# Optimization experiments

Hardware: AMD Instinct MI355X
Metric: run time of the kernel (lower is better)

The kernel has to match this reference:

```python
import jax, jax.numpy as jnp
import numpy as np

MARGIN = 0.5  # init kwarg margin=0.5 (float -> fix_margin branch)

N, D, NUM_CLASSES = 8192, 128, 512


def setup_inputs() -> dict:
    key = jax.random.key(0)
    k1, k2 = jax.random.split(key)
    embeds = jax.random.normal(k1, (N, D), dtype=jnp.float32)
    labels = jax.random.randint(k2, (N,), 0, NUM_CLASSES)
    return {"embeds": embeds, "labels": labels}


def reference(embeds, labels):
    n = embeds.shape[0]
    # --- batch-hard mining (detached in original: .detach().cpu().numpy()) ---
    # Euclidean pairwise distances via Gram trick (avoids [N,N,D] intermediate).
    sq = jnp.sum(embeds * embeds, axis=1)  # [N]
    d2 = sq[:, None] + sq[None, :] - 2.0 * (embeds @ embeds.T)  # [N,N]
    dist = jnp.sqrt(jnp.maximum(d2, 0.0))
    dist = jax.lax.stop_gradient(dist)

    same = labels[:, None] == labels[None, :]  # [N,N]
    eye = jnp.eye(n, dtype=bool)
    pos_mask = same & ~eye          # same label, not self
    neg_mask = ~same                # different label (diag excluded since same there)

    pos_idx = jnp.argmax(jnp.where(pos_mask, dist, -jnp.inf), axis=1)  # hardest positive
    neg_idx = jnp.argmin(jnp.where(neg_mask, dist, jnp.inf), axis=1)   # hardest negative

    # --- margin loss with metric='sqeuclidean' (gradients flow through gathers) ---
    dp = embeds - embeds[pos_idx]
    dn = embeds - embeds[neg_idx]
    ap = jnp.sum(dp * dp, axis=1)
    an = jnp.sum(dn * dn, axis=1)
    return jnp.mean(jax.nn.relu(ap - an + MARGIN))
```

## Files before the change

### kernel.cpp

```cpp
#include <hip/hip_runtime.h>
#include <stdint.h>

#define NROWS 8192
#define DIM 128
#define MARGIN 0.5f

typedef short short8 __attribute__((ext_vector_type(8)));
typedef float f32x4 __attribute__((ext_vector_type(4)));
typedef int   int4v __attribute__((ext_vector_type(4)));

static __device__ __forceinline__ unsigned short f2bf(float f) {
    union { float f; unsigned u; } x; x.f = f;
    unsigned u = x.u;
    return (unsigned short)((u + 0x7FFFu + ((u >> 16) & 1u)) >> 16);
}

__global__ __launch_bounds__(256) void prep(const float* __restrict__ emb,
                                            char* __restrict__ efrag,
                                            float* __restrict__ cbuf,
                                            unsigned* __restrict__ pos,
                                            unsigned* __restrict__ neg,
                                            float* __restrict__ out) {
    const int d = threadIdx.x & 63;
    const int row = blockIdx.x * 4 + (threadIdx.x >> 6);
    const float2 v = reinterpret_cast<const float2*>(emb + row * DIM)[d];
    float sq = v.x * v.x + v.y * v.y;
#pragma unroll
    for (int m = 1; m < 64; m <<= 1) sq += __shfl_xor(sq, m, 64);
    const unsigned pack = ((unsigned)f2bf(v.y) << 16) | (unsigned)f2bf(v.x);
    char* dst = efrag + (size_t)(row >> 4) * 4096 + (d >> 4) * 1024
              + ((((d >> 2) & 3) * 16 + (row & 15)) * 16) + (d & 3) * 4;
    *reinterpret_cast<unsigned*>(dst) = pack;
    if (d == 0) cbuf[row] = sq + 512.0f;
    if (d == 1) pos[row] = 0u;
    if (d == 2) neg[row] = 0xFFFFFFFFu;
    if (blockIdx.x == 0 && threadIdx.x == 0) out[0] = 0.0f;
}

__global__ __launch_bounds__(256, 4) void mine(const char* __restrict__ efrag,
                                               const float* __restrict__ cbuf,
                                               const int* __restrict__ labels,
                                               unsigned* __restrict__ pos,
                                               unsigned* __restrict__ neg) {
    const int tid  = threadIdx.x;
    const int wave = tid >> 6;
    const int lane = tid & 63;
    const int l15  = lane & 15;
    const int lhi  = lane >> 4;
    const int iblk = blockIdx.x & 31;
    const int cblk = blockIdx.x >> 5;
    const int ibase = iblk * 256 + wave * 64;

    short8 bfrag[4][4];
    int labi[4];
#pragma unroll
    for (int it = 0; it < 4; ++it) {
        const char* bt = efrag + (size_t)((ibase >> 4) + it) * 4096 + lane * 16;
#pragma unroll
        for (int ks = 0; ks < 4; ++ks)
            bfrag[it][ks] = *reinterpret_cast<const short8*>(bt + ks * 1024);
        labi[it] = labels[ibase + it * 16 + l15];
    }

    unsigned bp[4] = {0u, 0u, 0u, 0u};
    unsigned bn[4] = {0xFFFFFFFFu, 0xFFFFFFFFu, 0xFFFFFFFFu, 0xFFFFFFFFu};

    const int jc = cblk * 256;
    const char* aj = efrag + (size_t)(cblk * 16) * 4096 + lane * 16;

#pragma unroll 2
    for (int jt = 0; jt < 16; ++jt) {
        const int jb = jc + jt * 16;
        const int4v labj = *reinterpret_cast<const int4v*>(labels + jb + lhi * 4);
        const f32x4 cinit = *reinterpret_cast<const f32x4*>(cbuf + jb + lhi * 4) * -0.5f;
        const char* at = aj + (size_t)jt * 4096;

        const short8 af0 = *reinterpret_cast<const short8*>(at);
        const short8 af1 = *reinterpret_cast<const short8*>(at + 1024);
        f32x4 acc[4];
#pragma unroll
        for (int it = 0; it < 4; ++it)
            acc[it] = __builtin_amdgcn_mfma_f32_16x16x32_bf16(af0, bfrag[it][0], cinit, 0, 0, 0);
#pragma unroll
        for (int it = 0; it < 4; ++it)
            acc[it] = __builtin_amdgcn_mfma_f32_16x16x32_bf16(af1, bfrag[it][1], acc[it], 0, 0, 0);
        const short8 af2 = *reinterpret_cast<const short8*>(at + 2048);
        const short8 af3 = *reinterpret_cast<const short8*>(at + 3072);
#pragma unroll
        for (int it = 0; it < 4; ++it)
            acc[it] = __builtin_amdgcn_mfma_f32_16x16x32_bf16(af2, bfrag[it][2], acc[it], 0, 0, 0);
#pragma unroll
        for (int it = 0; it < 4; ++it)
            acc[it] = __builtin_amdgcn_mfma_f32_16x16x32_bf16(af3, bfrag[it][3], acc[it], 0, 0, 0);

        const int jv = jb + lhi * 4;
#pragma unroll
        for (int it = 0; it < 4; ++it) {
#pragma unroll
            for (int r = 0; r < 4; ++r) {
                union { float f; unsigned u; } cv; cv.f = acc[it][r];
                const unsigned cand = (cv.u & 0xFFFFE000u) | (unsigned)(jv + r);
                const bool eq = (labj[r] == labi[it]);
                const unsigned psel = eq ? cand : 0u;
                const unsigned nsel = eq ? 0xFFFFFFFFu : cand;
                bp[it] = bp[it] > psel ? bp[it] : psel;
                bn[it] = bn[it] < nsel ? bn[it] : nsel;
            }
        }
    }

#pragma unroll
    for (int it = 0; it < 4; ++it) {
        unsigned o;
        o = (unsigned)__shfl_xor((int)bp[it], 16, 64); bp[it] = bp[it] > o ? bp[it] : o;
        o = (unsigned)__shfl_xor((int)bp[it], 32, 64); bp[it] = bp[it] > o ? bp[it] : o;
        o = (unsigned)__shfl_xor((int)bn[it], 16, 64); bn[it] = bn[it] < o ? bn[it] : o;
        o = (unsigned)__shfl_xor((int)bn[it], 32, 64); bn[it] = bn[it] < o ? bn[it] : o;
        if (lane < 16) {
            const int i = ibase + it * 16 + lane;
            atomicMax(&pos[i], bp[it]);
            atomicMin(&neg[i], bn[it]);
        }
    }
}

__global__ __launch_bounds__(256) void lossk(const float* __restrict__ emb,
                                             const unsigned* __restrict__ pos,
                                             const unsigned* __restrict__ neg,
                                             float* __restrict__ bsum) {
    __shared__ float wsum[4];
    const int tid = threadIdx.x, lane = tid & 63, wave = tid >> 6;
    const int i = blockIdx.x * 4 + wave;
    const int jp = (int)(pos[i] & 8191u);
    const int jn = (int)(neg[i] & 8191u);
    const float2 a = reinterpret_cast<const float2*>(emb + (size_t)i  * DIM)[lane];
    const float2 b = reinterpret_cast<const float2*>(emb + (size_t)jp * DIM)[lane];
    const float2 c = reinterpret_cast<const float2*>(emb + (size_t)jn * DIM)[lane];
    float dx = a.x - b.x, dy = a.y - b.y;
    const float ap = dx * dx + dy * dy;
    dx = a.x - c.x; dy = a.y - c.y;
    const float an = dx * dx + dy * dy;
    float s = ap - an;
#pragma unroll
    for (int m = 1; m < 64; m <<= 1) s += __shfl_xor(s, m, 64);
    if (lane == 0) wsum[wave] = fmaxf(s + MARGIN, 0.f);
    __syncthreads();
    if (tid == 0) bsum[blockIdx.x] = wsum[0] + wsum[1] + wsum[2] + wsum[3];
}

__global__ __launch_bounds__(256) void fin(const float* __restrict__ bsum,
                                           float* __restrict__ out) {
    __shared__ float wsum[4];
    const int tid = threadIdx.x, lane = tid & 63, wave = tid >> 6;
    float s = 0.f;
#pragma unroll
    for (int k = 0; k < 8; ++k) s += bsum[tid + k * 256];
#pragma unroll
    for (int m = 1; m < 64; m <<= 1) s += __shfl_xor(s, m, 64);
    if (lane == 0) wsum[wave] = s;
    __syncthreads();
    if (tid == 0) out[0] = (wsum[0] + wsum[1] + wsum[2] + wsum[3]) * (1.0f / (float)NROWS);
}

extern "C" void kernel_launch(void* const* d_in, const int* in_sizes, int n_in,
                              void* d_out, int out_size, void* d_ws, size_t ws_size,
                              hipStream_t stream) {
    const float* emb   = (const float*)d_in[0];
    const int* labels  = (const int*)d_in[1];
    float* out = (float*)d_out;
    char* ws = (char*)d_ws;

    char* efrag    = ws;
    float* cbuf    = (float*)(ws + (size_t)2097152);
    unsigned* pos  = (unsigned*)(ws + (size_t)2097152 + 32768);
    unsigned* neg  = pos + NROWS;
    float* bsum    = (float*)(neg + NROWS);

    prep<<<2048, 256, 0, stream>>>(emb, efrag, cbuf, pos, neg, out);
    mine<<<1024, 256, 0, stream>>>(efrag, cbuf, labels, pos, neg);
    lossk<<<2048, 256, 0, stream>>>(emb, pos, neg, bsum);
    fin<<<1, 256, 0, stream>>>(bsum, out);
}
```

Baseline: 90.36 us.

## Sort rows by label so most tiles skip label compare and positive mining

Adds a histogram, a scan and a scatter that sort rows by label, then builds the bf16 fragments in that sorted order. Tile pairs whose column block cannot contain a same-label row go to a fast kernel that only tracks the minimum distance for negatives. Only the few diagonal-band tiles run the full label-aware kernel, and the loss maps indices back through the permutation. This cuts the per-element compare/select work across most of the N×N matrix, but adds four small launches, three of them single-block or tiny serial kernels, plus an indirection. Its correctness depends on each 256-row block's label range spanning at most three column blocks.

```diff
diff --git a/kernel.cpp b/kernel.cpp
--- a/kernel.cpp
+++ b/kernel.cpp
@@ -3,6 +3,7 @@
 
 #define NROWS 8192
 #define DIM 128
+#define NCLASS 512
 #define MARGIN 0.5f
 
 typedef short short8 __attribute__((ext_vector_type(8)));
@@ -14,41 +15,180 @@
     unsigned u = x.u;
     return (unsigned short)((u + 0x7FFFu + ((u >> 16) & 1u)) >> 16);
 }
-
-__global__ __launch_bounds__(256) void prep(const float* __restrict__ emb,
-                                            char* __restrict__ efrag,
-                                            float* __restrict__ cbuf,
-                                            unsigned* __restrict__ pos,
-                                            unsigned* __restrict__ neg,
+static __device__ __forceinline__ unsigned fbits(float f) {
+    union { float f; unsigned u; } x; x.f = f; return x.u;
+}
+
+__global__ __launch_bounds__(1024) void hist(const int* __restrict__ labels,
+                                             unsigned* __restrict__ bins) {
+    __shared__ unsigned h[NCLASS];
+    const int t = threadIdx.x;
+    if (t < NCLASS) h[t] = 0u;
+    __syncthreads();
+#pragma unroll
+    for (int k = 0; k < 8; ++k) atomicAdd(&h[labels[t + k * 1024]], 1u);
+    __syncthreads();
+    if (t < NCLASS) bins[t] = h[t];
+}
+
+__global__ __launch_bounds__(512) void scan(const unsigned* __restrict__ bins,
+                                            unsigned* __restrict__ binstart,
+                                            unsigned* __restrict__ cursor,
                                             float* __restrict__ out) {
+    __shared__ unsigned s[NCLASS];
+    const int t = threadIdx.x;
+    const unsigned v = bins[t];
+    s[t] = v;
+    __syncthreads();
+    for (int off = 1; off < NCLASS; off <<= 1) {
+        const unsigned x = (t >= off) ? s[t - off] : 0u;
+        __syncthreads();
+        s[t] += x;
+        __syncthreads();
+    }
+    const unsigned excl = s[t] - v;
+    binstart[t] = excl;
+    cursor[t] = excl;
+    if (t == 0) out[0] = 0.0f;
+}
+
+__global__ __launch_bounds__(256) void scatterk(const int* __restrict__ labels,
+                                                unsigned* __restrict__ cursor,
+                                                int* __restrict__ perm) {
+    const int i = blockIdx.x * 256 + threadIdx.x;
+    const unsigned p = atomicAdd(&cursor[labels[i]], 1u);
+    perm[p] = i;
+}
+
+__global__ __launch_bounds__(256) void build(const float* __restrict__ emb,
+                                             const int* __restrict__ labels,
+                                             const int* __restrict__ perm,
+                                             const unsigned* __restrict__ bins,
+                                             const unsigned* __restrict__ binstart,
+                                             char* __restrict__ efrag,
+                                             float* __restrict__ cs,
+                                             unsigned* __restrict__ pos,
+                                             unsigned* __restrict__ neg,
+                                             unsigned* __restrict__ rA,
+                                             unsigned* __restrict__ rB,
+                                             int* __restrict__ slab) {
     const int d = threadIdx.x & 63;
-    const int row = blockIdx.x * 4 + (threadIdx.x >> 6);
-    const float2 v = reinterpret_cast<const float2*>(emb + row * DIM)[d];
+    const int p = blockIdx.x * 4 + (threadIdx.x >> 6);
+    const int src = perm[p];
+    const float2 v = reinterpret_cast<const float2*>(emb + (size_t)src * DIM)[d];
     float sq = v.x * v.x + v.y * v.y;
 #pragma unroll
     for (int m = 1; m < 64; m <<= 1) sq += __shfl_xor(sq, m, 64);
     const unsigned pack = ((unsigned)f2bf(v.y) << 16) | (unsigned)f2bf(v.x);
-    char* dst = efrag + (size_t)(row >> 4) * 4096 + (d >> 4) * 1024
-              + ((((d >> 2) & 3) * 16 + (row & 15)) * 16) + (d & 3) * 4;
+    char* dst = efrag + (size_t)(p >> 4) * 4096 + (d >> 4) * 1024
+              + ((((d >> 2) & 3) * 16 + (p & 15)) * 16) + (d & 3) * 4;
     *reinterpret_cast<unsigned*>(dst) = pack;
-    if (d == 0) cbuf[row] = sq + 512.0f;
-    if (d == 1) pos[row] = 0u;
-    if (d == 2) neg[row] = 0xFFFFFFFFu;
-    if (blockIdx.x == 0 && threadIdx.x == 0) out[0] = 0.0f;
-}
-
-__global__ __launch_bounds__(256, 4) void mine(const char* __restrict__ efrag,
-                                               const float* __restrict__ cbuf,
-                                               const int* __restrict__ labels,
-                                               unsigned* __restrict__ pos,
-                                               unsigned* __restrict__ neg) {
+    const int lab = labels[src];
+    if (d == 0) cs[p] = sq + 512.0f;
+    if (d == 1) pos[p] = 0u;
+    if (d == 2) neg[p] = 0xFFFFFFFFu;
+    if (d == 3) rA[p] = binstart[lab];
+    if (d == 4) rB[p] = binstart[lab] + bins[lab];
+    if (d == 5) slab[p] = lab;
+}
+
+__global__ __launch_bounds__(256, 4) void mine_fast(const char* __restrict__ efrag,
+                                                    const float* __restrict__ cs,
+                                                    const unsigned* __restrict__ rA,
+                                                    const unsigned* __restrict__ rB,
+                                                    unsigned* __restrict__ neg) {
+    const int iblk = blockIdx.x & 31;
+    const int cblk = blockIdx.x >> 5;
+    const unsigned wlo = rA[iblk * 256];
+    const unsigned whi = rB[iblk * 256 + 255];
+    const int cba = (int)(wlo >> 8), cbb = (int)((whi - 1u) >> 8);
+    if (cblk >= cba && cblk <= cbb) return;
+
+    const int tid  = threadIdx.x;
+    const int wave = tid >> 6;
+    const int lane = tid & 63;
+    const int lhi  = lane >> 4;
+    const int ibase = iblk * 256 + wave * 64;
+
+    short8 bfrag[4][4];
+#pragma unroll
+    for (int it = 0; it < 4; ++it) {
+        const char* bt = efrag + (size_t)((ibase >> 4) + it) * 4096 + lane * 16;
+#pragma unroll
+        for (int ks = 0; ks < 4; ++ks)
+            bfrag[it][ks] = *reinterpret_cast<const short8*>(bt + ks * 1024);
+    }
+
+    unsigned bn[4] = {0xFFFFFFFFu, 0xFFFFFFFFu, 0xFFFFFFFFu, 0xFFFFFFFFu};
+    const int jc = cblk * 256;
+    const char* aj = efrag + (size_t)(cblk * 16) * 4096 + lane * 16;
+
+#pragma unroll 2
+    for (int jt = 0; jt < 16; ++jt) {
+        const int jb = jc + jt * 16;
+        const f32x4 cinit = *reinterpret_cast<const f32x4*>(cs + jb + lhi * 4) * -0.5f;
+        const char* at = aj + (size_t)jt * 4096;
+
+        const short8 af0 = *reinterpret_cast<const short8*>(at);
+        const short8 af1 = *reinterpret_cast<const short8*>(at + 1024);
+        f32x4 acc[4];
+#pragma unroll
+        for (int it = 0; it < 4; ++it)
+            acc[it] = __builtin_amdgcn_mfma_f32_16x16x32_bf16(af0, bfrag[it][0], cinit, 0, 0, 0);
+#pragma unroll
+        for (int it = 0; it < 4; ++it)
+            acc[it] = __builtin_amdgcn_mfma_f32_16x16x32_bf16(af1, bfrag[it][1], acc[it], 0, 0, 0);
+        const short8 af2 = *reinterpret_cast<const short8*>(at + 2048);
+        const short8 af3 = *reinterpret_cast<const short8*>(at + 3072);
+#pragma unroll
+        for (int it = 0; it < 4; ++it)
+            acc[it] = __builtin_amdgcn_mfma_f32_16x16x32_bf16(af2, bfrag[it][2], acc[it], 0, 0, 0);
+#pragma unroll
+        for (int it = 0; it < 4; ++it)
+            acc[it] = __builtin_amdgcn_mfma_f32_16x16x32_bf16(af3, bfrag[it][3], acc[it], 0, 0, 0);
+
+        const unsigned jv = (unsigned)(jb + lhi * 4);
+#pragma unroll
+        for (int it = 0; it < 4; ++it) {
+            const unsigned c0 = (fbits(acc[it][0]) & 0xFFFFE000u) | jv;
+            const unsigned c1 = (fbits(acc[it][1]) & 0xFFFFE000u) | (jv + 1u);
+            const unsigned c2 = (fbits(acc[it][2]) & 0xFFFFE000u) | (jv + 2u);
+            const unsigned c3 = (fbits(acc[it][3]) & 0xFFFFE000u) | (jv + 3u);
+            const unsigned m0 = c0 < c1 ? c0 : c1;
+            const unsigned m1 = c2 < c3 ? c2 : c3;
+            const unsigned m  = m0 < m1 ? m0 : m1;
+            bn[it] = bn[it] < m ? bn[it] : m;
+        }
+    }
+
+#pragma unroll
+    for (int it = 0; it < 4; ++it) {
+        unsigned o;
+        o = (unsigned)__shfl_xor((int)bn[it], 16, 64); bn[it] = bn[it] < o ? bn[it] : o;
+        o = (unsigned)__shfl_xor((int)bn[it], 32, 64); bn[it] = bn[it] < o ? bn[it] : o;
+        if (lane < 16) atomicMin(&neg[ibase + it * 16 + lane], bn[it]);
+    }
+}
+
+__global__ __launch_bounds__(256, 4) void mine_slow(const char* __restrict__ efrag,
+                                                    const float* __restrict__ cs,
+                                                    const int* __restrict__ slab,
+                                                    const unsigned* __restrict__ rA,
+                                                    const unsigned* __restrict__ rB,
+                                                    unsigned* __restrict__ pos,
+                                                    unsigned* __restrict__ neg) {
+    const int iblk = blockIdx.x;
+    const unsigned wlo = rA[iblk * 256];
+    const unsigned whi = rB[iblk * 256 + 255];
+    const int cba = (int)(wlo >> 8), cbb = (int)((whi - 1u) >> 8);
+    int cblk = cba + (int)blockIdx.y;
+    if (cblk > cbb) cblk = cbb;
+
     const int tid  = threadIdx.x;
     const int wave = tid >> 6;
     const int lane = tid & 63;
     const int l15  = lane & 15;
     const int lhi  = lane >> 4;
-    const int iblk = blockIdx.x & 31;
-    const int cblk = blockIdx.x >> 5;
     const int ibase = iblk * 256 + wave * 64;
 
     short8 bfrag[4][4];
@@ -59,20 +199,19 @@
 #pragma unroll
         for (int ks = 0; ks < 4; ++ks)
             bfrag[it][ks] = *reinterpret_cast<const short8*>(bt + ks * 1024);
-        labi[it] = labels[ibase + it * 16 + l15];
+        labi[it] = slab[ibase + it * 16 + l15];
     }
 
     unsigned bp[4] = {0u, 0u, 0u, 0u};
     unsigned bn[4] = {0xFFFFFFFFu, 0xFFFFFFFFu, 0xFFFFFFFFu, 0xFFFFFFFFu};
-
     const int jc = cblk * 256;
     const char* aj = efrag + (size_t)(cblk * 16) * 4096 + lane * 16;
 
 #pragma unroll 2
     for (int jt = 0; jt < 16; ++jt) {
         const int jb = jc + jt * 16;
-        const int4v labj = *reinterpret_cast<const int4v*>(labels + jb + lhi * 4);
-        const f32x4 cinit = *reinterpret_cast<const f32x4*>(cbuf + jb + lhi * 4) * -0.5f;
+        const int4v labj = *reinterpret_cast<const int4v*>(slab + jb + lhi * 4);
+        const f32x4 cinit = *reinterpret_cast<const f32x4*>(cs + jb + lhi * 4) * -0.5f;
         const char* at = aj + (size_t)jt * 4096;
 
         const short8 af0 = *reinterpret_cast<const short8*>(at);
@@ -98,8 +237,7 @@
         for (int it = 0; it < 4; ++it) {
 #pragma unroll
             for (int r = 0; r < 4; ++r) {
-                union { float f; unsigned u; } cv; cv.f = acc[it][r];
-                const unsigned cand = (cv.u & 0xFFFFE000u) | (unsigned)(jv + r);
+                const unsigned cand = (fbits(acc[it][r]) & 0xFFFFE000u) | (unsigned)(jv + r);
                 const bool eq = (labj[r] == labi[it]);
                 const unsigned psel = eq ? cand : 0u;
                 const unsigned nsel = eq ? 0xFFFFFFFFu : cand;
@@ -125,15 +263,17 @@
 }
 
 __global__ __launch_bounds__(256) void lossk(const float* __restrict__ emb,
+                                             const int* __restrict__ perm,
                                              const unsigned* __restrict__ pos,
                                              const unsigned* __restrict__ neg,
                                              float* __restrict__ bsum) {
     __shared__ float wsum[4];
     const int tid = threadIdx.x, lane = tid & 63, wave = tid >> 6;
     const int i = blockIdx.x * 4 + wave;
-    const int jp = (int)(pos[i] & 8191u);
-    const int jn = (int)(neg[i] & 8191u);
-    const float2 a = reinterpret_cast<const float2*>(emb + (size_t)i  * DIM)[lane];
+    const int pi = perm[i];
+    const int jp = perm[pos[i] & 8191u];
+    const int jn = perm[neg[i] & 8191u];
+    const float2 a = reinterpret_cast<const float2*>(emb + (size_t)pi * DIM)[lane];
     const float2 b = reinterpret_cast<const float2*>(emb + (size_t)jp * DIM)[lane];
     const float2 c = reinterpret_cast<const float2*>(emb + (size_t)jn * DIM)[lane];
     float dx = a.x - b.x, dy = a.y - b.y;
@@ -170,14 +310,26 @@
     float* out = (float*)d_out;
     char* ws = (char*)d_ws;
 
-    char* efrag    = ws;
-    float* cbuf    = (float*)(ws + (size_t)2097152);
-    unsigned* pos  = (unsigned*)(ws + (size_t)2097152 + 32768);
-    unsigned* neg  = pos + NROWS;
-    float* bsum    = (float*)(neg + NROWS);
-
-    prep<<<2048, 256, 0, stream>>>(emb, efrag, cbuf, pos, neg, out);
-    mine<<<1024, 256, 0, stream>>>(efrag, cbuf, labels, pos, neg);
-    lossk<<<2048, 256, 0, stream>>>(emb, pos, neg, bsum);
-    fin<<<1, 256, 0, stream>>>(bsum, out);
-}
+    char*     efrag    = ws;
+    float*    cs       = (float*)   (ws + 2097152);
+    unsigned* pos      = (unsigned*)(ws + 2129920);
+    unsigned* neg      = (unsigned*)(ws + 2162688);
+    float*    bsum     = (float*)   (ws + 2195456);
+    unsigned* bins     = (unsigned*)(ws + 2203648);
+    unsigned* binstart = (unsigned*)(ws + 2205696);
+    unsigned* cursor   = (unsigned*)(ws + 2207744);
+    int*      perm     = (int*)     (ws + 2209792);
+    unsigned* rA       = (unsigned*)(ws + 2242560);
+    unsigned* rB       = (unsigned*)(ws + 2275328);
+    int*      slab     = (int*)     (ws + 2308096);
+
+    hist    <<<1, 1024, 0, stream>>>(labels, bins);
+    scan    <<<1, 512, 0, stream>>>(bins, binstart, cursor, out);
+    scatterk<<<32, 256, 0, stream>>>(labels, cursor, perm);
+    build   <<<2048, 256, 0, stream>>>(emb, labels, perm, bins, binstart,
+                                       efrag, cs, pos, neg, rA, rB, slab);
+    mine_fast<<<1024, 256, 0, stream>>>(efrag, cs, rA, rB, neg);
+    mine_slow<<<dim3(32, 3), 256, 0, stream>>>(efrag, cs, slab, rA, rB, pos, neg);
+    lossk   <<<2048, 256, 0, stream>>>(emb, perm, pos, neg, bsum);
+    fin     <<<1, 256, 0, stream>>>(bsum, out);
+}
```

Result: slower. 108.8 us (+20.4%).
